# Kernel tuning notes

Measured on AMD Instinct MI355X. Metric: run time of the kernel, lower is better.

The kernel has to match this reference:

```python
import jax, jax.numpy as jnp
import numpy as np
from jax import lax

THETA = 1.0      # neuron['theta']
TAU_SR = 10.0    # neuron['tauSr'] (SRM synaptic time constant)
TAU_RHO = 1.0    # surrogate-gradient width
SCALE_RHO = 1.0  # surrogate-gradient scale
T_SIM = 100      # simulation['tSample']


def srm_kernel(T, dtype=jnp.float32):
    t = jnp.arange(T, dtype=dtype)
    return (t / TAU_SR) * jnp.exp(1.0 - t / TAU_SR)  # eps(0)=0, peak 1 at t=tau


def psp(x, eps):
    """Causal temporal filter along last axis: y[t] = sum_k eps[k] * x[t-k]."""
    shape = x.shape
    T = shape[-1]
    xf = x.reshape(-1, 1, T)
    k = eps[::-1].reshape(1, 1, T)
    y = lax.conv_general_dilated(xf, k, (1,), [(T - 1, 0)],
                                 dimension_numbers=('NCH', 'OIH', 'NCH'))
    return y.reshape(shape)


def spike(u):
    return (u >= THETA).astype(u.dtype)


def conv_t(x, w, pad):
    """Per-timestep 2D conv. x:[B,C,H,W,T], w:[O,I,kh,kw] -> [B,O,H',W',T]."""
    B, C, H, W, T = x.shape
    xt = jnp.moveaxis(x, -1, 1).reshape(B * T, C, H, W)
    y = lax.conv_general_dilated(xt, w, (1, 1), [(pad, pad), (pad, pad)],
                                 dimension_numbers=('NCHW', 'OIHW', 'NCHW'))
    O, Ho, Wo = y.shape[1], y.shape[2], y.shape[3]
    return jnp.moveaxis(y.reshape(B, T, O, Ho, Wo), 1, -1)


def pool2(x):
    """SLAYER pool: 2x2 sum with fixed weight 1.1. x:[B,C,H,W,T]."""
    B, C, H, W, T = x.shape
    xr = x.reshape(B, C, H // 2, 2, W // 2, 2, T)
    return 1.1 * xr.sum(axis=(3, 5))


def dense_t(x, w):
    """x:[B,C,H,W,T] flattened over CHW; w:[O, C*H*W] -> [B,O,T]."""
    B = x.shape[0]
    T = x.shape[-1]
    xf = x.reshape(B, -1, T)
    return jnp.einsum('bit,oi->bot', xf, w)


def setup_inputs() -> dict:
    key = jax.random.key(0)
    k = jax.random.split(key, 6)
    img = jax.random.uniform(k[0], (32, 1, 28, 28), dtype=jnp.float32)
    rand_u = jax.random.uniform(k[1], (32, 1, 28, 28, T_SIM), dtype=jnp.float32)
    w1 = jax.random.normal(k[2], (16, 1, 5, 5), dtype=jnp.float32) * 0.2
    w2 = jax.random.normal(k[3], (32, 16, 5, 5), dtype=jnp.float32) * 0.05
    wf1 = jax.random.normal(k[4], (410, 1568), dtype=jnp.float32) * 0.05
    wf2 = jax.random.normal(k[5], (10, 410), dtype=jnp.float32) * 0.05
    return {"img": img, "rand_u": rand_u, "w1": w1, "w2": w2, "wf1": wf1, "wf2": wf2}


def reference(img, rand_u, w1, w2, wf1, wf2):
    eps = srm_kernel(T_SIM, img.dtype)
    # rate encoding: Bernoulli spikes with p = pixel intensity
    x = (rand_u < img[..., None]).astype(img.dtype)          # [B,1,28,28,T]
    x = spike(psp(conv_t(x, w1, 2), eps))                    # [B,16,28,28,T]
    x = spike(psp(pool2(x), eps))                            # [B,16,14,14,T]
    x = spike(psp(conv_t(x, w2, 2), eps))                    # [B,32,14,14,T]
    x = spike(psp(pool2(x), eps))                            # [B,32,7,7,T]
    x = spike(psp(dense_t(x, wf1), eps))                     # [B,410,T]
    x = spike(psp(jnp.einsum('bit,oi->bot', x, wf2), eps))   # [B,10,T]
    return x
```

## Files before the change

### kernel.cpp

```cpp
#include <hip/hip_runtime.h>


namespace {
constexpr int B = 32, T = 100;
constexpr double A1 = 0.90483741803595957;
constexpr double CE = 0.27182818284590452;
constexpr double SC39 = 549755813888.0;
constexpr double INV39 = 1.0 / 549755813888.0;

constexpr size_t OFF_M1 = 0;
constexpr size_t OFF_M2 = OFF_M1 + (size_t)B * T * 28 * 4;
constexpr size_t OFF_S4 = OFF_M2 + (size_t)B * T * 224 * 4;
constexpr size_t OFF_D5 = OFF_S4 + (size_t)B * T * 1568;
constexpr size_t OFF_S5 = OFF_D5 + (size_t)B * T * 410 * 8;
constexpr size_t OFF_D6 = OFF_S5 + (size_t)B * T * 410;
constexpr size_t OFF_BP = OFF_D6 + (size_t)B * T * 10 * 8;
constexpr size_t OFF_AP = OFF_D5;
}

using i32x4 = __attribute__((ext_vector_type(4))) int;
using i32x16 = __attribute__((ext_vector_type(16))) int;

__global__ void k_encode_pack(const float* __restrict__ img, const float* __restrict__ ru,
                              unsigned int* __restrict__ m1) {
  int i = blockIdx.x * 256 + threadIdx.x;
  if (i >= B * 28 * T) return;
  int t = i % T;
  int y = (i / T) % 28;
  int b = i / (T * 28);
  unsigned int m = 0;
  const float* rb = ru + ((size_t)b * 784 + y * 28) * T + t;
  const float* ib = img + b * 784 + y * 28;
  for (int x = 0; x < 28; x++) {
    m |= (rb[(size_t)x * T] < ib[x]) ? (1u << x) : 0u;
  }
  m1[((size_t)b * T + t) * 28 + y] = m;
}

__global__ __launch_bounds__(256) void k_conv1(const unsigned int* __restrict__ m1,
                                               const float* __restrict__ w1,
                                               unsigned int* __restrict__ m2) {
  __shared__ double lut[160];
  __shared__ unsigned int mrow[2][32];
  __shared__ unsigned char spk[784];
  __shared__ unsigned char spkP[2][196];
  int o = blockIdx.x % 16, b = blockIdx.x / 16;
  int tid = threadIdx.x;
  if (tid < 160) {
    int dy = tid / 32, f = tid % 32;
    double v = 0.0;
    const float* wb = w1 + o * 25 + dy * 5;
#pragma unroll
    for (int dx = 0; dx < 5; dx++)
      if ((f >> dx) & 1) v += (double)wb[dx];
    lut[tid] = v;
  }
  if (tid < 32) {
    mrow[0][tid] = 0;
    mrow[1][tid] = 0;
  }
  int y = tid / 7, xg = tid % 7;
  int py = tid / 14, px = tid % 14;
  bool act = tid < 196;
  double g1[4] = {0, 0, 0, 0}, g2[4] = {0, 0, 0, 0};
  double p1 = 0.0, p2 = 0.0;
  const unsigned int* m1b = m1 + (size_t)b * T * 28;
  if (tid < 28) mrow[0][tid + 2] = m1b[tid] << 2;
  __syncthreads();
  for (int t = 0; t < T; t++) {
    int cur = t & 1, nxt = cur ^ 1;
    bool dold = (tid < 28) && (t + 1 < T);
    unsigned int ldv = 0;
    if (dold) ldv = m1b[(t + 1) * 28 + tid] << 2;
    if (act) {
      double s0 = 0, s1 = 0, s2 = 0, s3 = 0;
      int xb = xg * 4;
      const unsigned int* mc = mrow[cur];
#pragma unroll
      for (int dy = 0; dy < 5; dy++) {
        unsigned int m = mc[y + dy];
        const double* ld = lut + dy * 32;
        s0 += ld[(m >> (xb + 0)) & 31];
        s1 += ld[(m >> (xb + 1)) & 31];
        s2 += ld[(m >> (xb + 2)) & 31];
        s3 += ld[(m >> (xb + 3)) & 31];
      }
      g1[0] = s0 + A1 * g1[0]; g2[0] = g1[0] + A1 * g2[0];
      g1[1] = s1 + A1 * g1[1]; g2[1] = g1[1] + A1 * g2[1];
      g1[2] = s2 + A1 * g1[2]; g2[2] = g1[2] + A1 * g2[2];
      g1[3] = s3 + A1 * g1[3]; g2[3] = g1[3] + A1 * g2[3];
      unsigned char* sp = spk + y * 28 + xb;
      sp[0] = (CE * (g2[0] - g1[0]) >= 1.0) ? 1 : 0;
      sp[1] = (CE * (g2[1] - g1[1]) >= 1.0) ? 1 : 0;
      sp[2] = (CE * (g2[2] - g1[2]) >= 1.0) ? 1 : 0;
      sp[3] = (CE * (g2[3] - g1[3]) >= 1.0) ? 1 : 0;
    }
    if (dold) mrow[nxt][tid + 2] = ldv;
    __syncthreads();
    if (act) {
      const unsigned char* r0 = spk + (2 * py) * 28 + 2 * px;
      int sum = (int)r0[0] + (int)r0[1] + (int)r0[28] + (int)r0[29];
      double s = 1.1 * (double)sum;
      p1 = s + A1 * p1;
      p2 = p1 + A1 * p2;
      spkP[cur][tid] = (CE * (p2 - p1) >= 1.0) ? 1 : 0;
    }
    if (tid < 14 && t > 0) {
      unsigned int m = 0;
      const unsigned char* rp = spkP[nxt] + tid * 14;
#pragma unroll
      for (int xx = 0; xx < 14; xx++) m |= ((unsigned int)rp[xx]) << xx;
      m2[((size_t)(b * T + (t - 1)) * 16 + o) * 14 + tid] = m;
    }
    __syncthreads();
  }
  if (tid < 14) {
    unsigned int m = 0;
    const unsigned char* rp = spkP[(T - 1) & 1] + tid * 14;
#pragma unroll
    for (int xx = 0; xx < 14; xx++) m |= ((unsigned int)rp[xx]) << xx;
    m2[((size_t)(b * T + (T - 1)) * 16 + o) * 14 + tid] = m;
  }
}

__global__ void k_limbs(const float* __restrict__ w2, signed char* __restrict__ AP) {
  int i = blockIdx.x * 256 + threadIdx.x;
  if (i >= 32 * 80 * 8) return;
  int dx = i & 7;
  int g = (i >> 3) % 80;
  int o = i / 640;
  int c = g >> 2, r = g & 3, eh = r >> 1, kh = r & 1;
  int lane = kh * 32 + o, e = eh * 8 + dx;
  int ci = g / 5, dy = g % 5;
  float wv = (dx < 5) ? w2[((o * 16 + ci) * 5 + dy) * 5 + dx] : 0.0f;
  long long m = llrint((double)wv * SC39);
#pragma unroll
  for (int j = 0; j < 5; j++) {
    int d = (int)((m + 128) & 255) - 128;
    AP[(size_t)((j * 20 + c) * 64 + lane) * 16 + e] = (signed char)d;
    m = (m - d) >> 8;
  }
}

__global__ __launch_bounds__(512, 2) void k_conv2w(const unsigned int* __restrict__ m2,
                                                   const signed char* __restrict__ AP,
                                                   unsigned char* __restrict__ s4) {
  __shared__ unsigned int maskW[2][2][192];
  __shared__ double part[2][4][32][30];
  int yp = blockIdx.x % 7, b = blockIdx.x / 7;
  int y0 = yp * 2;
  int tid = threadIdx.x;
  int w = tid >> 6, l = tid & 63;
  int tp = w & 1, kq = w >> 1;
  int col = l & 31, kh = l >> 5;
  int x = col % 14;
  unsigned int wmask = (col < 28) ? 31u : 0u;
  int half = (col >= 14) ? 1 : 0;
  const unsigned int* m2b = m2 + (size_t)b * T * 224;

  const i32x4* APv = (const i32x4*)AP;
  i32x4 Af[5][5];
#pragma unroll
  for (int j = 0; j < 5; j++)
#pragma unroll
    for (int q = 0; q < 5; q++)
      Af[j][q] = APv[(size_t)(j * 20 + 5 * kq + q) * 64 + l];

  int stPos[3] = {-1, -1, -1}, stIdx[3] = {-1, -1, -1};
  if (w < 2) {
#pragma unroll
    for (int pass = 0; pass < 3; pass++) {
      if (pass == 2 && l >= 32) continue;
      int e = pass * 64 + l;
      int H = e / 80, g = e % 80;
      int c = g >> 2, eh2 = (g >> 1) & 1, kh2 = g & 1;
      int kq2 = c / 5, q2 = c % 5;
      int ci = g / 5, dy = g % 5;
      int iy = y0 - 2 + H + dy;
      stPos[pass] = H * 96 + kh2 * 48 + kq2 * 12 + q2 * 2 + eh2;
      if (iy >= 0 && iy < 14) stIdx[pass] = ci * 14 + iy;
    }
  }

  int ct = tid - 256;
  bool chainAct = (ct >= 0) && (ct < 224);
  int po = (ct >= 0) ? ct / 7 : 0;
  int pp = (ct >= 0) ? ct % 7 : 0;
  double sg1[4] = {0, 0, 0, 0}, sg2[4] = {0, 0, 0, 0};
  double pq1 = 0.0, pq2 = 0.0;

  if (w < 2) {
#pragma unroll
    for (int pass = 0; pass < 3; pass++) {
      if (stPos[pass] < 0) continue;
      unsigned int v = 0;
      if (stIdx[pass] >= 0) v = m2b[(size_t)w * 224 + stIdx[pass]] << 2;
      maskW[0][w][stPos[pass]] = v;
    }
  }
  __syncthreads();

  for (int grp = 0; grp < 50; grp++) {
    int p = grp & 1, np = p ^ 1;

    unsigned int ld0 = 0, ld1 = 0, ld2 = 0;
    bool doStage = (w < 2) && (grp + 1 < 50);
    if (doStage) {
      size_t tb = (size_t)((grp + 1) * 2 + w) * 224;
      if (stIdx[0] >= 0) ld0 = m2b[tb + stIdx[0]] << 2;
      if (stIdx[1] >= 0) ld1 = m2b[tb + stIdx[1]] << 2;
      if (stIdx[2] >= 0) ld2 = m2b[tb + stIdx[2]] << 2;
    }

    {
      const uint4* mwv = (const uint4*)&maskW[p][tp][0];
      int base4 = half * 24 + kh * 12 + kq * 3;
      uint4 mk0 = mwv[base4 + 0], mk1 = mwv[base4 + 1], mk2 = mwv[base4 + 2];
      i32x16 ac0, ac1, ac2, ac3, ac4;
#pragma unroll
      for (int r = 0; r < 16; r++) { ac0[r] = 0; ac1[r] = 0; ac2[r] = 0; ac3[r] = 0; ac4[r] = 0; }
#pragma unroll
      for (int q = 0; q < 5; q++) {
        unsigned int ra = (q == 0) ? mk0.x : (q == 1) ? mk0.z : (q == 2) ? mk1.x
                         : (q == 3) ? mk1.z : mk2.x;
        unsigned int rb = (q == 0) ? mk0.y : (q == 1) ? mk0.w : (q == 2) ? mk1.y
                         : (q == 3) ? mk1.w : mk2.y;
        unsigned int a5 = (ra >> x) & wmask;
        unsigned int b5 = (rb >> x) & wmask;
        i32x4 bb;
        bb[0] = (int)(((a5 & 15u) * 0x204081u) & 0x01010101u);
        bb[1] = (int)((a5 >> 4) & 1u);
        bb[2] = (int)(((b5 & 15u) * 0x204081u) & 0x01010101u);
        bb[3] = (int)((b5 >> 4) & 1u);
        ac0 = __builtin_amdgcn_mfma_i32_32x32x32_i8(Af[0][q], bb, ac0, 0, 0, 0);
        ac1 = __builtin_amdgcn_mfma_i32_32x32x32_i8(Af[1][q], bb, ac1, 0, 0, 0);
        ac2 = __builtin_amdgcn_mfma_i32_32x32x32_i8(Af[2][q], bb, ac2, 0, 0, 0);
        ac3 = __builtin_amdgcn_mfma_i32_32x32x32_i8(Af[3][q], bb, ac3, 0, 0, 0);
        ac4 = __builtin_amdgcn_mfma_i32_32x32x32_i8(Af[4][q], bb, ac4, 0, 0, 0);
      }
      if (col < 28) {
#pragma unroll
        for (int r = 0; r < 16; r++) {
          int R = (r & 3) + 8 * (r >> 2) + 4 * kh;
          int c01 = ac1[r] * 256 + ac0[r];
          int c23 = ac3[r] * 256 + ac2[r];
          double S = ((double)ac4[r] * 65536.0 + (double)c23) * 65536.0 + (double)c01;
          part[tp][kq][R][col] = S;
        }
      }
    }

    if (doStage) {
      if (stPos[0] >= 0) maskW[np][w][stPos[0]] = ld0;
      if (stPos[1] >= 0) maskW[np][w][stPos[1]] = ld1;
      if (stPos[2] >= 0) maskW[np][w][stPos[2]] = ld2;
    }
    __syncthreads();

    if (chainAct) {
#pragma unroll
      for (int g = 0; g < 2; g++) {
        const double* q0a = &part[g][0][po][2 * pp];
        const double* q1a = &part[g][1][po][2 * pp];
        const double* q2a = &part[g][2][po][2 * pp];
        const double* q3a = &part[g][3][po][2 * pp];
        const double* q0b = &part[g][0][po][14 + 2 * pp];
        const double* q1b = &part[g][1][po][14 + 2 * pp];
        const double* q2b = &part[g][2][po][14 + 2 * pp];
        const double* q3b = &part[g][3][po][14 + 2 * pp];
        double c0 = ((q0a[0] + q1a[0]) + (q2a[0] + q3a[0])) * INV39;
        double c1 = ((q0a[1] + q1a[1]) + (q2a[1] + q3a[1])) * INV39;
        double c2 = ((q0b[0] + q1b[0]) + (q2b[0] + q3b[0])) * INV39;
        double c3 = ((q0b[1] + q1b[1]) + (q2b[1] + q3b[1])) * INV39;
        sg1[0] = c0 + A1 * sg1[0]; sg2[0] = sg1[0] + A1 * sg2[0];
        sg1[1] = c1 + A1 * sg1[1]; sg2[1] = sg1[1] + A1 * sg2[1];
        sg1[2] = c2 + A1 * sg1[2]; sg2[2] = sg1[2] + A1 * sg2[2];
        sg1[3] = c3 + A1 * sg1[3]; sg2[3] = sg1[3] + A1 * sg2[3];
        int sum = ((CE * (sg2[0] - sg1[0]) >= 1.0) ? 1 : 0)
                + ((CE * (sg2[1] - sg1[1]) >= 1.0) ? 1 : 0)
                + ((CE * (sg2[2] - sg1[2]) >= 1.0) ? 1 : 0)
                + ((CE * (sg2[3] - sg1[3]) >= 1.0) ? 1 : 0);
        double s = 1.1 * (double)sum;
        pq1 = s + A1 * pq1;
        pq2 = pq1 + A1 * pq2;
        s4[(size_t)(b * T + grp * 2 + g) * 1568 + po * 49 + yp * 7 + pp] =
            (CE * (pq2 - pq1) >= 1.0) ? 1 : 0;
      }
    }
    __syncthreads();
  }
}

__global__ void k_limbs2(const float* __restrict__ wf1, signed char* __restrict__ BP) {
  int i = blockIdx.x * 256 + threadIdx.x;
  if (i >= 13 * 5 * 49 * 64) return;
  int lane = i & 63;
  int fi = i >> 6;
  int c = fi % 49;
  int j = (fi / 49) % 5;
  int ot = fi / 245;
  int o = ot * 32 + (lane & 31);
  int kb = 32 * c + (lane >> 5) * 16;
  int wd[4] = {0, 0, 0, 0};
#pragma unroll
  for (int e = 0; e < 16; e++) {
    float wv = (o < 410) ? wf1[(size_t)o * 1568 + kb + e] : 0.0f;
    long long m = llrint((double)wv * SC39);
    int d = 0;
    for (int jj = 0; jj <= j; jj++) {
      d = (int)((m + 128) & 255) - 128;
      m = (m - d) >> 8;
    }
    wd[e >> 2] |= (d & 255) << ((e & 3) * 8);
  }
  i32x4 v;
  v[0] = wd[0]; v[1] = wd[1]; v[2] = wd[2]; v[3] = wd[3];
  *(i32x4*)(BP + (size_t)i * 16) = v;
}

__global__ __launch_bounds__(256) void k_dense1m(const unsigned char* __restrict__ s4,
                                                 const signed char* __restrict__ BP,
                                                 double* __restrict__ d5) {
  int ot = blockIdx.y;
  int w = threadIdx.x >> 6, l = threadIdx.x & 63;
  int col = l & 31, kh = l >> 5;
  int btTile = blockIdx.x * 4 + w;
  const unsigned char* arow = s4 + (size_t)(btTile * 32 + col) * 1568 + kh * 16;
  const i32x4* bpv = (const i32x4*)BP + (size_t)ot * 245 * 64 + l;
  i32x16 acc0, acc1, acc2, acc3, acc4;
#pragma unroll
  for (int r = 0; r < 16; r++) {
    acc0[r] = 0; acc1[r] = 0; acc2[r] = 0; acc3[r] = 0; acc4[r] = 0;
  }
  for (int c = 0; c < 49; c++) {
    i32x4 a = *(const i32x4*)(arow + 32 * c);
    i32x4 b0 = bpv[(0 * 49 + c) * 64];
    i32x4 b1 = bpv[(1 * 49 + c) * 64];
    i32x4 b2 = bpv[(2 * 49 + c) * 64];
    i32x4 b3 = bpv[(3 * 49 + c) * 64];
    i32x4 b4 = bpv[(4 * 49 + c) * 64];
    acc0 = __builtin_amdgcn_mfma_i32_32x32x32_i8(a, b0, acc0, 0, 0, 0);
    acc1 = __builtin_amdgcn_mfma_i32_32x32x32_i8(a, b1, acc1, 0, 0, 0);
    acc2 = __builtin_amdgcn_mfma_i32_32x32x32_i8(a, b2, acc2, 0, 0, 0);
    acc3 = __builtin_amdgcn_mfma_i32_32x32x32_i8(a, b3, acc3, 0, 0, 0);
    acc4 = __builtin_amdgcn_mfma_i32_32x32x32_i8(a, b4, acc4, 0, 0, 0);
  }
  int o = ot * 32 + col;
  if (o < 410) {
#pragma unroll
    for (int r = 0; r < 16; r++) {
      int R = (r & 3) + 8 * (r >> 2) + 4 * kh;
      double v = ((((double)acc4[r] * 256.0 + (double)acc3[r]) * 256.0 +
                   (double)acc2[r]) * 256.0 + (double)acc1[r]) * 256.0 + (double)acc0[r];
      d5[(size_t)(btTile * 32 + R) * 410 + o] = v * INV39;
    }
  }
}

__global__ void k_psp5(const double* __restrict__ d5, unsigned char* __restrict__ s5) {
  int tid = blockIdx.x * 256 + threadIdx.x;
  if (tid >= B * 410) return;
  int o = tid % 410, b = tid / 410;
  double g1 = 0.0, g2 = 0.0;
  for (int t = 0; t < T; t++) {
    double s = d5[(size_t)(b * T + t) * 410 + o];
    g1 = s + A1 * g1;
    g2 = g1 + A1 * g2;
    s5[(size_t)(b * T + t) * 410 + o] = (CE * (g2 - g1) >= 1.0) ? 1 : 0;
  }
}

__global__ void k_dense2(const unsigned char* __restrict__ s5, const float* __restrict__ wf2,
                         double* __restrict__ d6) {
  int tid = blockIdx.x * 256 + threadIdx.x;
  if (tid >= B * T * 10) return;
  int o = tid % 10, bt = tid / 10;
  const unsigned char* sr = s5 + (size_t)bt * 410;
  const float* wr = wf2 + o * 410;
  double s = 0.0;
  for (int i = 0; i < 410; i++) s += (double)wr[i] * (double)sr[i];
  d6[tid] = s;
}

__global__ void k_psp6(const double* __restrict__ d6, float* __restrict__ out) {
  int tid = blockIdx.x * 256 + threadIdx.x;
  if (tid >= B * 10) return;
  int o = tid % 10, b = tid / 10;
  double g1 = 0.0, g2 = 0.0;
  for (int t = 0; t < T; t++) {
    double s = d6[(size_t)(b * T + t) * 10 + o];
    g1 = s + A1 * g1;
    g2 = g1 + A1 * g2;
    out[(size_t)b * 1000 + o * 100 + t] = (CE * (g2 - g1) >= 1.0) ? 1.0f : 0.0f;
  }
}

extern "C" void kernel_launch(void* const* d_in, const int* in_sizes, int n_in,
                              void* d_out, int out_size, void* d_ws, size_t ws_size,
                              hipStream_t stream) {
  const float* img = (const float*)d_in[0];
  const float* ru = (const float*)d_in[1];
  const float* w1 = (const float*)d_in[2];
  const float* w2 = (const float*)d_in[3];
  const float* wf1 = (const float*)d_in[4];
  const float* wf2 = (const float*)d_in[5];

  unsigned char* ws = (unsigned char*)d_ws;
  unsigned int* m1 = (unsigned int*)(ws + OFF_M1);
  unsigned int* m2 = (unsigned int*)(ws + OFF_M2);
  unsigned char* s4 = ws + OFF_S4;
  double* d5 = (double*)(ws + OFF_D5);
  unsigned char* s5 = ws + OFF_S5;
  double* d6 = (double*)(ws + OFF_D6);
  signed char* AP = (signed char*)(ws + OFF_AP);
  signed char* BP = (signed char*)(ws + OFF_BP);
  float* out = (float*)d_out;

  k_encode_pack<<<(B * 28 * T + 255) / 256, 256, 0, stream>>>(img, ru, m1);
  k_limbs<<<(32 * 80 * 8 + 255) / 256, 256, 0, stream>>>(w2, AP);
  k_limbs2<<<(13 * 5 * 49 * 64 + 255) / 256, 256, 0, stream>>>(wf1, BP);
  k_conv1<<<B * 16, 256, 0, stream>>>(m1, w1, m2);
  k_conv2w<<<B * 7, 512, 0, stream>>>(m2, AP, s4);
  k_dense1m<<<dim3(25, 13), 256, 0, stream>>>(s4, BP, d5);
  k_psp5<<<(B * 410 + 255) / 256, 256, 0, stream>>>(d5, s5);
  k_dense2<<<(B * T * 10 + 255) / 256, 256, 0, stream>>>(s5, wf2, d6);
  k_psp6<<<2, 256, 0, stream>>>(d6, out);
}
```

Baseline: 376.0 us.

## Fuse conv1 spike and 2x2 pool in registers with ballot bit-packing

Remaps conv1 threads so each thread owns a 2x2 output quad, which lets the pool and its PSP be computed in registers instead of through a shared spike buffer. Pooled spikes are packed into row bitmasks with a wavefront ballot, removing one of the two block barriers per timestep and the serial byte-packing loop. A 64-entry lookup table returning two adjacent weight sums halves the number of LUT lookups. The change relies on 64-wide wavefronts (16 columns per row fits lane&48) and uses a larger shared LUT.

```diff
diff --git a/kernel.cpp b/kernel.cpp
--- a/kernel.cpp
+++ b/kernel.cpp
@@ -37,89 +37,79 @@
   m1[((size_t)b * T + t) * 28 + y] = m;
 }
 
-__global__ __launch_bounds__(256) void k_conv1(const unsigned int* __restrict__ m1,
-                                               const float* __restrict__ w1,
-                                               unsigned int* __restrict__ m2) {
-  __shared__ double lut[160];
+__global__ __launch_bounds__(256) void k_conv1w(const unsigned int* __restrict__ m1,
+                                                const float* __restrict__ w1,
+                                                unsigned int* __restrict__ m2) {
+  __shared__ double lut2[320 * 2];
   __shared__ unsigned int mrow[2][32];
-  __shared__ unsigned char spk[784];
-  __shared__ unsigned char spkP[2][196];
   int o = blockIdx.x % 16, b = blockIdx.x / 16;
   int tid = threadIdx.x;
-  if (tid < 160) {
-    int dy = tid / 32, f = tid % 32;
-    double v = 0.0;
+  for (int e = tid; e < 320; e += 256) {
+    int dy = e / 64, f = e % 64;
     const float* wb = w1 + o * 25 + dy * 5;
-#pragma unroll
-    for (int dx = 0; dx < 5; dx++)
-      if ((f >> dx) & 1) v += (double)wb[dx];
-    lut[tid] = v;
+    double v0 = 0.0, v1 = 0.0;
+#pragma unroll
+    for (int dx = 0; dx < 5; dx++) {
+      double wv = (double)wb[dx];
+      if ((f >> dx) & 1) v0 += wv;
+      if ((f >> (dx + 1)) & 1) v1 += wv;
+    }
+    lut2[e * 2 + 0] = v0;
+    lut2[e * 2 + 1] = v1;
   }
   if (tid < 32) {
     mrow[0][tid] = 0;
     mrow[1][tid] = 0;
   }
-  int y = tid / 7, xg = tid % 7;
-  int py = tid / 14, px = tid % 14;
-  bool act = tid < 196;
+  int py = tid >> 4, px = tid & 15;
+  bool act = (px < 14) && (py < 14);
+  int yA = 2 * py, xA = 2 * px;
   double g1[4] = {0, 0, 0, 0}, g2[4] = {0, 0, 0, 0};
-  double p1 = 0.0, p2 = 0.0;
+  double q1 = 0.0, q2 = 0.0;
   const unsigned int* m1b = m1 + (size_t)b * T * 28;
   if (tid < 28) mrow[0][tid + 2] = m1b[tid] << 2;
   __syncthreads();
   for (int t = 0; t < T; t++) {
-    int cur = t & 1, nxt = cur ^ 1;
+    int p = t & 1, np = p ^ 1;
     bool dold = (tid < 28) && (t + 1 < T);
     unsigned int ldv = 0;
     if (dold) ldv = m1b[(t + 1) * 28 + tid] << 2;
+    unsigned int poolBit = 0;
     if (act) {
-      double s0 = 0, s1 = 0, s2 = 0, s3 = 0;
-      int xb = xg * 4;
-      const unsigned int* mc = mrow[cur];
+      double sAa = 0, sAb = 0, sBa = 0, sBb = 0;
+      const unsigned int* mc = mrow[p];
 #pragma unroll
       for (int dy = 0; dy < 5; dy++) {
-        unsigned int m = mc[y + dy];
-        const double* ld = lut + dy * 32;
-        s0 += ld[(m >> (xb + 0)) & 31];
-        s1 += ld[(m >> (xb + 1)) & 31];
-        s2 += ld[(m >> (xb + 2)) & 31];
-        s3 += ld[(m >> (xb + 3)) & 31];
+        unsigned int mA = mc[yA + dy];
+        unsigned int mB = mc[yA + 1 + dy];
+        const double* eA = lut2 + (dy * 64 + (int)((mA >> xA) & 63u)) * 2;
+        const double* eB = lut2 + (dy * 64 + (int)((mB >> xA) & 63u)) * 2;
+        sAa += eA[0];
+        sAb += eA[1];
+        sBa += eB[0];
+        sBb += eB[1];
       }
-      g1[0] = s0 + A1 * g1[0]; g2[0] = g1[0] + A1 * g2[0];
-      g1[1] = s1 + A1 * g1[1]; g2[1] = g1[1] + A1 * g2[1];
-      g1[2] = s2 + A1 * g1[2]; g2[2] = g1[2] + A1 * g2[2];
-      g1[3] = s3 + A1 * g1[3]; g2[3] = g1[3] + A1 * g2[3];
-      unsigned char* sp = spk + y * 28 + xb;
-      sp[0] = (CE * (g2[0] - g1[0]) >= 1.0) ? 1 : 0;
-      sp[1] = (CE * (g2[1] - g1[1]) >= 1.0) ? 1 : 0;
-      sp[2] = (CE * (g2[2] - g1[2]) >= 1.0) ? 1 : 0;
-      sp[3] = (CE * (g2[3] - g1[3]) >= 1.0) ? 1 : 0;
-    }
-    if (dold) mrow[nxt][tid + 2] = ldv;
+      g1[0] = sAa + A1 * g1[0]; g2[0] = g1[0] + A1 * g2[0];
+      g1[1] = sAb + A1 * g1[1]; g2[1] = g1[1] + A1 * g2[1];
+      g1[2] = sBa + A1 * g1[2]; g2[2] = g1[2] + A1 * g2[2];
+      g1[3] = sBb + A1 * g1[3]; g2[3] = g1[3] + A1 * g2[3];
+      int s0 = (CE * (g2[0] - g1[0]) >= 1.0) ? 1 : 0;
+      int s1 = (CE * (g2[1] - g1[1]) >= 1.0) ? 1 : 0;
+      int s2 = (CE * (g2[2] - g1[2]) >= 1.0) ? 1 : 0;
+      int s3 = (CE * (g2[3] - g1[3]) >= 1.0) ? 1 : 0;
+      double s = 1.1 * (double)(s0 + s1 + s2 + s3);
+      q1 = s + A1 * q1;
+      q2 = q1 + A1 * q2;
+      poolBit = (CE * (q2 - q1) >= 1.0) ? 1u : 0u;
+    }
+    unsigned long long bal = __ballot((int)poolBit);
+    if (act && px == 0) {
+      int lane = tid & 63;
+      unsigned int rm = (unsigned int)((bal >> (lane & 48)) & 0x3FFFull);
+      m2[((size_t)(b * T + t) * 16 + o) * 14 + py] = rm;
+    }
+    if (dold) mrow[np][tid + 2] = ldv;
     __syncthreads();
-    if (act) {
-      const unsigned char* r0 = spk + (2 * py) * 28 + 2 * px;
-      int sum = (int)r0[0] + (int)r0[1] + (int)r0[28] + (int)r0[29];
-      double s = 1.1 * (double)sum;
-      p1 = s + A1 * p1;
-      p2 = p1 + A1 * p2;
-      spkP[cur][tid] = (CE * (p2 - p1) >= 1.0) ? 1 : 0;
-    }
-    if (tid < 14 && t > 0) {
-      unsigned int m = 0;
-      const unsigned char* rp = spkP[nxt] + tid * 14;
-#pragma unroll
-      for (int xx = 0; xx < 14; xx++) m |= ((unsigned int)rp[xx]) << xx;
-      m2[((size_t)(b * T + (t - 1)) * 16 + o) * 14 + tid] = m;
-    }
-    __syncthreads();
-  }
-  if (tid < 14) {
-    unsigned int m = 0;
-    const unsigned char* rp = spkP[(T - 1) & 1] + tid * 14;
-#pragma unroll
-    for (int xx = 0; xx < 14; xx++) m |= ((unsigned int)rp[xx]) << xx;
-    m2[((size_t)(b * T + (T - 1)) * 16 + o) * 14 + tid] = m;
   }
 }
 
@@ -419,7 +409,7 @@
   k_encode_pack<<<(B * 28 * T + 255) / 256, 256, 0, stream>>>(img, ru, m1);
   k_limbs<<<(32 * 80 * 8 + 255) / 256, 256, 0, stream>>>(w2, AP);
   k_limbs2<<<(13 * 5 * 49 * 64 + 255) / 256, 256, 0, stream>>>(wf1, BP);
-  k_conv1<<<B * 16, 256, 0, stream>>>(m1, w1, m2);
+  k_conv1w<<<B * 16, 256, 0, stream>>>(m1, w1, m2);
   k_conv2w<<<B * 7, 512, 0, stream>>>(m2, AP, s4);
   k_dense1m<<<dim3(25, 13), 256, 0, stream>>>(s4, BP, d5);
   k_psp5<<<(B * 410 + 255) / 256, 256, 0, stream>>>(d5, s5);
```

Measured after the change: 353.5 us. 6.0% less time.
